# Kernel optimization log

Measured on AMD Instinct MI355X. Metric: run time of the kernel, lower is better.

Reference implementation:

```python
import jax, jax.numpy as jnp
import numpy as np

B, T, S, U, VOCAB = 32, 64, 64, 512, 65


def setup_inputs() -> dict:
    key = jax.random.key(0)
    ks = jax.random.split(key, 16)
    sd = 0.05
    return {
        "shifted_labels": jax.random.randint(ks[0], (B, T), 0, VOCAB),
        "encoder_output": jax.random.normal(ks[1], (B, S, U), jnp.float32),
        "enc_state_h": jax.random.normal(ks[2], (B, U), jnp.float32),
        "enc_state_c": jax.random.normal(ks[3], (B, U), jnp.float32),
        # decoder LSTM params (keras gate order i,f,g,o)
        "Wx": jax.random.normal(ks[4], (VOCAB, 4 * U), jnp.float32) * sd,
        "Wh": jax.random.normal(ks[5], (U, 4 * U), jnp.float32) * sd,
        "b": jnp.zeros((4 * U,), jnp.float32),
        # Bahdanau attention params
        "W1": jax.random.normal(ks[6], (U, U), jnp.float32) * sd,
        "b1": jnp.zeros((U,), jnp.float32),
        "W2": jax.random.normal(ks[7], (U, U), jnp.float32) * sd,
        "b2": jnp.zeros((U,), jnp.float32),
        "V": jax.random.normal(ks[8], (U, 1), jnp.float32) * sd,
        "bv": jnp.zeros((1,), jnp.float32),
    }


def _lstm(xz, h0, c0, Wh):
    # xz: [B, T, 4U] precomputed input projections
    def step(carry, xz_t):
        h, c = carry
        z = xz_t + h @ Wh
        i, f, g, o = jnp.split(z, 4, axis=-1)
        c = jax.nn.sigmoid(f) * c + jax.nn.sigmoid(i) * jnp.tanh(g)
        h = jax.nn.sigmoid(o) * jnp.tanh(c)
        return (h, c), h

    (_, _), hs = jax.lax.scan(step, (h0, c0), jnp.swapaxes(xz, 0, 1))
    return jnp.swapaxes(hs, 0, 1)  # [B, T, U]


def reference(shifted_labels, encoder_output, enc_state_h, enc_state_c,
              Wx, Wh, b, W1, b1, W2, b2, V, bv):
    vocab = Wx.shape[0]
    x = jax.nn.one_hot(shifted_labels, vocab, dtype=encoder_output.dtype)  # [B,T,vocab]
    xz = jnp.einsum('btv,vk->btk', x, Wx) + b                              # [B,T,4U]
    dec = _lstm(xz, enc_state_h, enc_state_c, Wh)                          # [B,T,U]
    # Bahdanau attention, vectorized over all decoder timesteps at once
    d1 = dec @ W1 + b1                # [B,T,U]
    e2 = encoder_output @ W2 + b2     # [B,S,U]  (computed once, not per step)
    score = jnp.tanh(d1[:, :, None, :] + e2[:, None, :, :]) @ V + bv  # [B,T,S,1]
    w = jax.nn.softmax(score[..., 0], axis=-1)  # softmax over encoder positions S
    return jnp.transpose(w, (0, 2, 1))          # [B,S,T] (stack axis=2 in original)
```

## Files before the change

kernel.cpp:

```cpp
#include <hip/hip_runtime.h>
#include <hip/hip_bf16.h>


#define NB 32
#define NT 64
#define NS 64
#define NU 512
#define N4U 2048
#define NV 65
#define NWG 32

typedef unsigned int u32;
typedef __bf16 bf16_t;
typedef bf16_t bf16x8 __attribute__((ext_vector_type(8)));
typedef float f32x4 __attribute__((ext_vector_type(4)));
typedef u32 u32x4 __attribute__((ext_vector_type(4)));

__device__ __forceinline__ unsigned short f2bf(float f) {
  u32 u = __builtin_bit_cast(u32, f);
  u += 0x7fffu + ((u >> 16) & 1u);
  return (unsigned short)(u >> 16);
}
__device__ __forceinline__ float bf2f(unsigned short s) {
  return __builtin_bit_cast(float, (u32)s << 16);
}
__device__ __forceinline__ u32 pk2(float a, float b) {
  return (u32)f2bf(a) | ((u32)f2bf(b) << 16);
}
__device__ __forceinline__ float sigf(float x) { return 1.0f / (1.0f + __expf(-x)); }
__device__ __forceinline__ float tanhfast(float x) {
  float e = __expf(2.0f * x);
  return 1.0f - 2.0f / (e + 1.0f);
}

__global__ __launch_bounds__(256, 1)
void lstm_kernel(const int* __restrict__ labels,
                 const float* __restrict__ h0,
                 const float* __restrict__ c0,
                 const float* __restrict__ Wx,
                 const float* __restrict__ Wh,
                 const float* __restrict__ bias,
                 const float* __restrict__ enc,
                 const float* __restrict__ W2,
                 const float* __restrict__ b2,
                 u32* __restrict__ hbuf,
                 u32* __restrict__ dec_u,
                 u32* __restrict__ flags,
                 unsigned short* __restrict__ e2_bf)
{
  __shared__ float z_buf[NB][65];
  __shared__ float c_lds[NB][16];
  __shared__ float wx_lds[NV][65];
  __shared__ unsigned char lab_lds[NB * NT];

  const int tid  = threadIdx.x;
  const int g    = blockIdx.x;
  const int wave = tid >> 6, lane = tid & 63;
  const int l15  = lane & 15, l4 = lane >> 4;

  if (g >= NWG) {
    const int r0 = (g - NWG) * 64 + wave * 16;
    const int arowE = r0 + l15;
    u32x4 afragE[16];
#pragma unroll
    for (int kt = 0; kt < 16; ++kt) {
      const float* ep = enc + arowE * NU + kt * 32 + l4 * 8;
      u32x4 t;
      t.x = pk2(ep[0], ep[1]); t.y = pk2(ep[2], ep[3]);
      t.z = pk2(ep[4], ep[5]); t.w = pk2(ep[6], ep[7]);
      afragE[kt] = t;
    }
    for (int cg = 0; cg < 8; ++cg) {
      f32x4 acc[4] = {};
      for (int kt = 0; kt < 16; ++kt) {
        bf16x8 a = __builtin_bit_cast(bf16x8, afragE[kt]);
        int k0 = kt * 32 + l4 * 8;
#pragma unroll
        for (int nt = 0; nt < 4; ++nt) {
          int col = cg * 64 + nt * 16 + l15;
          union { unsigned short us[8]; bf16x8 v; } bu;
#pragma unroll
          for (int e = 0; e < 8; ++e) bu.us[e] = f2bf(W2[(k0 + e) * NU + col]);
          acc[nt] = __builtin_amdgcn_mfma_f32_16x16x32_bf16(a, bu.v, acc[nt], 0, 0, 0);
        }
      }
#pragma unroll
      for (int nt = 0; nt < 4; ++nt) {
        int col = cg * 64 + nt * 16 + l15;
        float bc = b2[col];
#pragma unroll
        for (int ri = 0; ri < 4; ++ri)
          e2_bf[(r0 + l4 * 4 + ri) * NU + col] = f2bf(acc[nt][ri] + bc);
      }
    }
    return;
  }

  const int wm = wave >> 1, wn = wave & 1;

  for (int i = tid; i < NV * 64; i += 256) {
    int v = i >> 6, c = i & 63;
    int j = (c >> 4) * NU + g * 16 + (c & 15);
    wx_lds[v][c] = Wx[v * N4U + j] + bias[j];
  }
  for (int i = tid; i < NB * 16; i += 256) {
    int r = i >> 4, u = i & 15;
    c_lds[r][u] = c0[r * NU + g * 16 + u];
  }
  for (int i = tid; i < NB * NT; i += 256) lab_lds[i] = (unsigned char)labels[i];

  bf16x8 bfrag[16][2];
#pragma unroll
  for (int kt = 0; kt < 16; ++kt) {
#pragma unroll
    for (int nt = 0; nt < 2; ++nt) {
      int c = wn * 32 + nt * 16 + l15;
      int j = (c >> 4) * NU + g * 16 + (c & 15);
      int kb = kt * 32 + l4 * 8;
      union { unsigned short us[8]; bf16x8 v; } bu;
#pragma unroll
      for (int e = 0; e < 8; ++e) bu.us[e] = f2bf(Wh[(kb + e) * N4U + j]);
      bfrag[kt][nt] = bu.v;
    }
  }

  const int arow = wm * 16 + l15;
  u32x4 afrag[16];
#pragma unroll
  for (int kt = 0; kt < 16; ++kt) {
    const float* hp = h0 + arow * NU + kt * 32 + l4 * 8;
    u32x4 t;
    t.x = pk2(hp[0], hp[1]); t.y = pk2(hp[2], hp[3]);
    t.z = pk2(hp[4], hp[5]); t.w = pk2(hp[6], hp[7]);
    afrag[kt] = t;
  }

  const int bb = tid >> 3;
  const int u2 = (tid & 7) * 2;
  const int ci = g * 8 + (tid & 7);

  for (int s = 0; s < NT; ++s) {
    f32x4 a00 = {0.f,0.f,0.f,0.f}, a01 = a00, a10 = a00, a11 = a00;
#pragma unroll
    for (int kt = 0; kt < 16; kt += 2) {
      bf16x8 av0 = __builtin_bit_cast(bf16x8, afrag[kt]);
      bf16x8 av1 = __builtin_bit_cast(bf16x8, afrag[kt + 1]);
      a00 = __builtin_amdgcn_mfma_f32_16x16x32_bf16(av0, bfrag[kt][0],     a00, 0, 0, 0);
      a10 = __builtin_amdgcn_mfma_f32_16x16x32_bf16(av0, bfrag[kt][1],     a10, 0, 0, 0);
      a01 = __builtin_amdgcn_mfma_f32_16x16x32_bf16(av1, bfrag[kt + 1][0], a01, 0, 0, 0);
      a11 = __builtin_amdgcn_mfma_f32_16x16x32_bf16(av1, bfrag[kt + 1][1], a11, 0, 0, 0);
    }
    f32x4 acc0 = a00 + a01, acc1 = a10 + a11;

#pragma unroll
    for (int ri = 0; ri < 4; ++ri) {
      z_buf[wm * 16 + l4 * 4 + ri][wn * 32 + l15]      = acc0[ri];
      z_buf[wm * 16 + l4 * 4 + ri][wn * 32 + 16 + l15] = acc1[ri];
    }
    __syncthreads();

    int lab = lab_lds[bb * NT + s];
    float hv[2];
#pragma unroll
    for (int q = 0; q < 2; ++q) {
      int u = u2 + q;
      float zi = z_buf[bb][u]      + wx_lds[lab][u];
      float zf = z_buf[bb][16 + u] + wx_lds[lab][16 + u];
      float zg = z_buf[bb][32 + u] + wx_lds[lab][32 + u];
      float zo = z_buf[bb][48 + u] + wx_lds[lab][48 + u];
      float cc = sigf(zf) * c_lds[bb][u] + sigf(zi) * tanhfast(zg);
      c_lds[bb][u] = cc;
      hv[q] = sigf(zo) * tanhfast(cc);
    }
    u32 pkv = pk2(hv[0], hv[1]);

    if (s == NT - 1) {
      dec_u[(bb * NT + s) * 256 + ci] = pkv;
      break;
    }

    __hip_atomic_store(hbuf + (((s + 1) & 1) << 13) + bb * 256 + ci, pkv,
                       __ATOMIC_RELAXED, __HIP_MEMORY_SCOPE_AGENT);

    asm volatile("s_waitcnt vmcnt(0)" ::: "memory");
    __syncthreads();

    if (tid == 0)
      __hip_atomic_store(flags + g, (u32)(s + 1),
                         __ATOMIC_RELAXED, __HIP_MEMORY_SCOPE_AGENT);

    dec_u[(bb * NT + s) * 256 + ci] = pkv;

    {
      const u32 target = (u32)(s + 1);
      int guard = 0;
      for (;;) {
        u32 f = target;
        if (lane < NWG)
          f = __hip_atomic_load(flags + lane, __ATOMIC_RELAXED,
                                __HIP_MEMORY_SCOPE_AGENT);
        if (__all(f >= target)) break;
        if (++guard > 300000) break;
        __builtin_amdgcn_s_sleep(1);
      }
    }

    {
      const u32* ap = hbuf + (((s + 1) & 1) << 13) + arow * 256 + l4 * 4;
      asm volatile(
        "global_load_dwordx4 %0, %16, off sc0 sc1\n\t"
        "global_load_dwordx4 %1, %16, off offset:64 sc0 sc1\n\t"
        "global_load_dwordx4 %2, %16, off offset:128 sc0 sc1\n\t"
        "global_load_dwordx4 %3, %16, off offset:192 sc0 sc1\n\t"
        "global_load_dwordx4 %4, %16, off offset:256 sc0 sc1\n\t"
        "global_load_dwordx4 %5, %16, off offset:320 sc0 sc1\n\t"
        "global_load_dwordx4 %6, %16, off offset:384 sc0 sc1\n\t"
        "global_load_dwordx4 %7, %16, off offset:448 sc0 sc1\n\t"
        "global_load_dwordx4 %8, %16, off offset:512 sc0 sc1\n\t"
        "global_load_dwordx4 %9, %16, off offset:576 sc0 sc1\n\t"
        "global_load_dwordx4 %10, %16, off offset:640 sc0 sc1\n\t"
        "global_load_dwordx4 %11, %16, off offset:704 sc0 sc1\n\t"
        "global_load_dwordx4 %12, %16, off offset:768 sc0 sc1\n\t"
        "global_load_dwordx4 %13, %16, off offset:832 sc0 sc1\n\t"
        "global_load_dwordx4 %14, %16, off offset:896 sc0 sc1\n\t"
        "global_load_dwordx4 %15, %16, off offset:960 sc0 sc1\n\t"
        "s_waitcnt vmcnt(0)"
        : "=&v"(afrag[0]),  "=&v"(afrag[1]),  "=&v"(afrag[2]),  "=&v"(afrag[3]),
          "=&v"(afrag[4]),  "=&v"(afrag[5]),  "=&v"(afrag[6]),  "=&v"(afrag[7]),
          "=&v"(afrag[8]),  "=&v"(afrag[9]),  "=&v"(afrag[10]), "=&v"(afrag[11]),
          "=&v"(afrag[12]), "=&v"(afrag[13]), "=&v"(afrag[14]), "=&v"(afrag[15])
        : "v"(ap)
        : "memory");
    }
  }
}

__global__ __launch_bounds__(256, 1)
void proj_kernel(const u32* __restrict__ dec_u,
                 const float* __restrict__ W1,
                 const float* __restrict__ b1,
                 unsigned short* __restrict__ d1_bf)
{
  const int tid = threadIdx.x;
  const int wave = tid >> 6, lane = tid & 63;
  const int l15 = lane & 15, l4 = lane >> 4;
  const int w  = blockIdx.x * 4 + wave;
  const int rt = w >> 3, cg = w & 7;
  const int r0 = rt * 16;

  f32x4 acc[4] = {};
  const int arow = r0 + l15;
  for (int kt = 0; kt < 16; ++kt) {
    int k0 = kt * 32 + l4 * 8;
    bf16x8 a = __builtin_bit_cast(bf16x8,
          *reinterpret_cast<const uint4*>(dec_u + arow * 256 + (k0 >> 1)));
#pragma unroll
    for (int nt = 0; nt < 4; ++nt) {
      int col = cg * 64 + nt * 16 + l15;
      union { unsigned short us[8]; bf16x8 v; } bu;
#pragma unroll
      for (int e = 0; e < 8; ++e) bu.us[e] = f2bf(W1[(k0 + e) * NU + col]);
      acc[nt] = __builtin_amdgcn_mfma_f32_16x16x32_bf16(a, bu.v, acc[nt], 0, 0, 0);
    }
  }
#pragma unroll
  for (int nt = 0; nt < 4; ++nt) {
    int col = cg * 64 + nt * 16 + l15;
    float bc = b1[col];
#pragma unroll
    for (int ri = 0; ri < 4; ++ri) {
      int row = r0 + l4 * 4 + ri;
      d1_bf[row * NU + col] = f2bf(acc[nt][ri] + bc);
    }
  }
}

__global__ __launch_bounds__(256, 1)
void score_kernel(const unsigned short* __restrict__ d1_bf,
                  const unsigned short* __restrict__ e2_bf,
                  const float* __restrict__ V,
                  float* __restrict__ out)
{
  const int tid = threadIdx.x;
  const int wave = tid >> 6, lane = tid & 63;
  const int p = blockIdx.x * 4 + wave;
  const int bb = p >> 6, t = p & 63;

  union { uint4 q; unsigned short us[8]; } dv;
  dv.q = *reinterpret_cast<const uint4*>(d1_bf + (bb * 64 + t) * NU + lane * 8);
  float d1f[8], Vf[8];
#pragma unroll
  for (int e = 0; e < 8; ++e) { d1f[e] = bf2f(dv.us[e]); Vf[e] = V[lane * 8 + e]; }

  float sc = 0.f;
  for (int s = 0; s < NS; ++s) {
    union { uint4 q; unsigned short us[8]; } ev;
    ev.q = *reinterpret_cast<const uint4*>(e2_bf + (bb * 64 + s) * NU + lane * 8);
    float part = 0.f;
#pragma unroll
    for (int e = 0; e < 8; ++e) part += tanhfast(d1f[e] + bf2f(ev.us[e])) * Vf[e];
#pragma unroll
    for (int o = 32; o > 0; o >>= 1) part += __shfl_xor(part, o);
    sc = (lane == s) ? part : sc;
  }
  float m = sc;
#pragma unroll
  for (int o = 32; o > 0; o >>= 1) m = fmaxf(m, __shfl_xor(m, o));
  float ex = __expf(sc - m);
  float sum = ex;
#pragma unroll
  for (int o = 32; o > 0; o >>= 1) sum += __shfl_xor(sum, o);
  out[(bb * 64 + lane) * 64 + t] = ex / sum;
}

extern "C" void kernel_launch(void* const* d_in, const int* in_sizes, int n_in,
                              void* d_out, int out_size, void* d_ws, size_t ws_size,
                              hipStream_t stream)
{
  (void)in_sizes; (void)n_in; (void)out_size;
  const int*   labels = (const int*)  d_in[0];
  const float* enc    = (const float*)d_in[1];
  const float* h0     = (const float*)d_in[2];
  const float* c0     = (const float*)d_in[3];
  const float* Wx     = (const float*)d_in[4];
  const float* Wh     = (const float*)d_in[5];
  const float* bias   = (const float*)d_in[6];
  const float* W1     = (const float*)d_in[7];
  const float* b1     = (const float*)d_in[8];
  const float* W2     = (const float*)d_in[9];
  const float* b2     = (const float*)d_in[10];
  const float* V      = (const float*)d_in[11];

  char* ws = (char*)d_ws;
  const size_t OFS_HBUF = 1024;
  const size_t OFS_DEC  = 1u << 17;
  const size_t OFS_D1   = OFS_DEC + (2u << 20);
  const size_t OFS_E2   = OFS_D1  + (2u << 20);
  if (ws_size < OFS_E2 + (2u << 20)) return;

  u32* flags = (u32*)(ws);
  u32* hbuf  = (u32*)(ws + OFS_HBUF);
  u32* dec_u = (u32*)(ws + OFS_DEC);
  unsigned short* d1_bf = (unsigned short*)(ws + OFS_D1);
  unsigned short* e2_bf = (unsigned short*)(ws + OFS_E2);
  float* out = (float*)d_out;

  hipMemsetAsync(flags, 0, 256, stream);
  lstm_kernel<<<dim3(64), dim3(256), 0, stream>>>(labels, h0, c0, Wx, Wh, bias,
                                                  enc, W2, b2,
                                                  hbuf, dec_u, flags, e2_bf);
  proj_kernel<<<dim3(256), dim3(256), 0, stream>>>(dec_u, W1, b1, d1_bf);
  score_kernel<<<dim3(512), dim3(256), 0, stream>>>(d1_bf, e2_bf, V, out);
}
```

Before: 384.1 us.

## Fuse W1 projection into idle LSTM helper workgroups, overlapping it with the recurrence

The separate proj_kernel launch is removed. The 32 helper workgroups that previously only computed e2 now also compute d1 = h_t @ W1 + b1 for each timestep. They poll the per-step flags and read h_t from a full-history hbuf that replaces the double-buffered one. This hides the projection behind the serial LSTM recurrence and saves a kernel launch plus the dec_u round trip. It costs a larger workspace, extra polling traffic on the flags that could slow the critical recurrence loop, and a tail where the helpers must finish the last step after the recurrence ends.

```diff
diff --git a/kernel.cpp b/kernel.cpp
--- a/kernel.cpp
+++ b/kernel.cpp
@@ -32,6 +32,32 @@
   float e = __expf(2.0f * x);
   return 1.0f - 2.0f / (e + 1.0f);
 }
+
+#define LOAD_HSLOT(DST, AP)                                                   \
+  asm volatile(                                                               \
+    "global_load_dwordx4 %0, %16, off sc0 sc1\n\t"                            \
+    "global_load_dwordx4 %1, %16, off offset:64 sc0 sc1\n\t"                  \
+    "global_load_dwordx4 %2, %16, off offset:128 sc0 sc1\n\t"                 \
+    "global_load_dwordx4 %3, %16, off offset:192 sc0 sc1\n\t"                 \
+    "global_load_dwordx4 %4, %16, off offset:256 sc0 sc1\n\t"                 \
+    "global_load_dwordx4 %5, %16, off offset:320 sc0 sc1\n\t"                 \
+    "global_load_dwordx4 %6, %16, off offset:384 sc0 sc1\n\t"                 \
+    "global_load_dwordx4 %7, %16, off offset:448 sc0 sc1\n\t"                 \
+    "global_load_dwordx4 %8, %16, off offset:512 sc0 sc1\n\t"                 \
+    "global_load_dwordx4 %9, %16, off offset:576 sc0 sc1\n\t"                 \
+    "global_load_dwordx4 %10, %16, off offset:640 sc0 sc1\n\t"                \
+    "global_load_dwordx4 %11, %16, off offset:704 sc0 sc1\n\t"                \
+    "global_load_dwordx4 %12, %16, off offset:768 sc0 sc1\n\t"                \
+    "global_load_dwordx4 %13, %16, off offset:832 sc0 sc1\n\t"                \
+    "global_load_dwordx4 %14, %16, off offset:896 sc0 sc1\n\t"                \
+    "global_load_dwordx4 %15, %16, off offset:960 sc0 sc1\n\t"                \
+    "s_waitcnt vmcnt(0)"                                                      \
+    : "=&v"(DST[0]),  "=&v"(DST[1]),  "=&v"(DST[2]),  "=&v"(DST[3]),          \
+      "=&v"(DST[4]),  "=&v"(DST[5]),  "=&v"(DST[6]),  "=&v"(DST[7]),          \
+      "=&v"(DST[8]),  "=&v"(DST[9]),  "=&v"(DST[10]), "=&v"(DST[11]),         \
+      "=&v"(DST[12]), "=&v"(DST[13]), "=&v"(DST[14]), "=&v"(DST[15])          \
+    : "v"(AP)                                                                 \
+    : "memory")
 
 __global__ __launch_bounds__(256, 1)
 void lstm_kernel(const int* __restrict__ labels,
@@ -43,9 +69,11 @@
                  const float* __restrict__ enc,
                  const float* __restrict__ W2,
                  const float* __restrict__ b2,
+                 const float* __restrict__ W1,
+                 const float* __restrict__ b1,
                  u32* __restrict__ hbuf,
-                 u32* __restrict__ dec_u,
                  u32* __restrict__ flags,
+                 unsigned short* __restrict__ d1_bf,
                  unsigned short* __restrict__ e2_bf)
 {
   __shared__ float z_buf[NB][65];
@@ -59,38 +87,84 @@
   const int l15  = lane & 15, l4 = lane >> 4;
 
   if (g >= NWG) {
-    const int r0 = (g - NWG) * 64 + wave * 16;
-    const int arowE = r0 + l15;
-    u32x4 afragE[16];
-#pragma unroll
-    for (int kt = 0; kt < 16; ++kt) {
-      const float* ep = enc + arowE * NU + kt * 32 + l4 * 8;
-      u32x4 t;
-      t.x = pk2(ep[0], ep[1]); t.y = pk2(ep[2], ep[3]);
-      t.z = pk2(ep[4], ep[5]); t.w = pk2(ep[6], ep[7]);
-      afragE[kt] = t;
-    }
-    for (int cg = 0; cg < 8; ++cg) {
-      f32x4 acc[4] = {};
+    const int k = g - NWG;
+    {
+      const int r0 = k * 64 + wave * 16;
+      const int arowE = r0 + l15;
+      u32x4 afragE[16];
+#pragma unroll
       for (int kt = 0; kt < 16; ++kt) {
-        bf16x8 a = __builtin_bit_cast(bf16x8, afragE[kt]);
-        int k0 = kt * 32 + l4 * 8;
+        const float* ep = enc + arowE * NU + kt * 32 + l4 * 8;
+        u32x4 t;
+        t.x = pk2(ep[0], ep[1]); t.y = pk2(ep[2], ep[3]);
+        t.z = pk2(ep[4], ep[5]); t.w = pk2(ep[6], ep[7]);
+        afragE[kt] = t;
+      }
+      for (int cg = 0; cg < 8; ++cg) {
+        f32x4 acc[4] = {};
+        for (int kt = 0; kt < 16; ++kt) {
+          bf16x8 a = __builtin_bit_cast(bf16x8, afragE[kt]);
+          int k0 = kt * 32 + l4 * 8;
+#pragma unroll
+          for (int nt = 0; nt < 4; ++nt) {
+            int col = cg * 64 + nt * 16 + l15;
+            union { unsigned short us[8]; bf16x8 v; } bu;
+#pragma unroll
+            for (int e = 0; e < 8; ++e) bu.us[e] = f2bf(W2[(k0 + e) * NU + col]);
+            acc[nt] = __builtin_amdgcn_mfma_f32_16x16x32_bf16(a, bu.v, acc[nt], 0, 0, 0);
+          }
+        }
 #pragma unroll
         for (int nt = 0; nt < 4; ++nt) {
           int col = cg * 64 + nt * 16 + l15;
-          union { unsigned short us[8]; bf16x8 v; } bu;
-#pragma unroll
-          for (int e = 0; e < 8; ++e) bu.us[e] = f2bf(W2[(k0 + e) * NU + col]);
-          acc[nt] = __builtin_amdgcn_mfma_f32_16x16x32_bf16(a, bu.v, acc[nt], 0, 0, 0);
+          float bc = b2[col];
+#pragma unroll
+          for (int ri = 0; ri < 4; ++ri)
+            e2_bf[(r0 + l4 * 4 + ri) * NU + col] = f2bf(acc[nt][ri] + bc);
         }
       }
-#pragma unroll
-      for (int nt = 0; nt < 4; ++nt) {
-        int col = cg * 64 + nt * 16 + l15;
-        float bc = b2[col];
-#pragma unroll
-        for (int ri = 0; ri < 4; ++ri)
-          e2_bf[(r0 + l4 * 4 + ri) * NU + col] = f2bf(acc[nt][ri] + bc);
+    }
+
+    {
+      const int wm = wave >> 1, wn = wave & 1;
+      const int col = k * 16 + l15;
+      const float bc1 = b1[col];
+      bf16x8 bfrag1[16];
+#pragma unroll
+      for (int kt = 0; kt < 16; ++kt) {
+        int kb = kt * 32 + l4 * 8;
+        union { unsigned short us[8]; bf16x8 v; } bu;
+#pragma unroll
+        for (int e = 0; e < 8; ++e) bu.us[e] = f2bf(W1[(kb + e) * NU + col]);
+        bfrag1[kt] = bu.v;
+      }
+      const int arow1 = wm * 16 + l15;
+      for (int t = 1 + wn; t <= NT; t += 2) {
+        {
+          int guard = 0;
+          for (;;) {
+            u32 f = (u32)t;
+            if (lane < NWG)
+              f = __hip_atomic_load(flags + lane, __ATOMIC_RELAXED,
+                                    __HIP_MEMORY_SCOPE_AGENT);
+            if (__all(f >= (u32)t)) break;
+            if (++guard > 2000000) break;
+            __builtin_amdgcn_s_sleep(2);
+          }
+        }
+        u32x4 hf[16];
+        const u32* ap1 = hbuf + (size_t)t * 8192 + arow1 * 256 + l4 * 4;
+        LOAD_HSLOT(hf, ap1);
+        f32x4 acc = {0.f, 0.f, 0.f, 0.f};
+#pragma unroll
+        for (int kt = 0; kt < 16; ++kt)
+          acc = __builtin_amdgcn_mfma_f32_16x16x32_bf16(
+                  __builtin_bit_cast(bf16x8, hf[kt]), bfrag1[kt], acc, 0, 0, 0);
+#pragma unroll
+        for (int ri = 0; ri < 4; ++ri) {
+          int b = wm * 16 + l4 * 4 + ri;
+          d1_bf[(b * NT + (t - 1)) * NU + col] = f2bf(acc[ri] + bc1);
+        }
       }
     }
     return;
@@ -174,12 +248,7 @@
     }
     u32 pkv = pk2(hv[0], hv[1]);
 
-    if (s == NT - 1) {
-      dec_u[(bb * NT + s) * 256 + ci] = pkv;
-      break;
-    }
-
-    __hip_atomic_store(hbuf + (((s + 1) & 1) << 13) + bb * 256 + ci, pkv,
+    __hip_atomic_store(hbuf + (size_t)(s + 1) * 8192 + bb * 256 + ci, pkv,
                        __ATOMIC_RELAXED, __HIP_MEMORY_SCOPE_AGENT);
 
     asm volatile("s_waitcnt vmcnt(0)" ::: "memory");
@@ -189,7 +258,7 @@
       __hip_atomic_store(flags + g, (u32)(s + 1),
                          __ATOMIC_RELAXED, __HIP_MEMORY_SCOPE_AGENT);
 
-    dec_u[(bb * NT + s) * 256 + ci] = pkv;
+    if (s == NT - 1) break;
 
     {
       const u32 target = (u32)(s + 1);
@@ -206,71 +275,8 @@
     }
 
     {
-      const u32* ap = hbuf + (((s + 1) & 1) << 13) + arow * 256 + l4 * 4;
-      asm volatile(
-        "global_load_dwordx4 %0, %16, off sc0 sc1\n\t"
-        "global_load_dwordx4 %1, %16, off offset:64 sc0 sc1\n\t"
-        "global_load_dwordx4 %2, %16, off offset:128 sc0 sc1\n\t"
-        "global_load_dwordx4 %3, %16, off offset:192 sc0 sc1\n\t"
-        "global_load_dwordx4 %4, %16, off offset:256 sc0 sc1\n\t"
-        "global_load_dwordx4 %5, %16, off offset:320 sc0 sc1\n\t"
-        "global_load_dwordx4 %6, %16, off offset:384 sc0 sc1\n\t"
-        "global_load_dwordx4 %7, %16, off offset:448 sc0 sc1\n\t"
-        "global_load_dwordx4 %8, %16, off offset:512 sc0 sc1\n\t"
-        "global_load_dwordx4 %9, %16, off offset:576 sc0 sc1\n\t"
-        "global_load_dwordx4 %10, %16, off offset:640 sc0 sc1\n\t"
-        "global_load_dwordx4 %11, %16, off offset:704 sc0 sc1\n\t"
-        "global_load_dwordx4 %12, %16, off offset:768 sc0 sc1\n\t"
-        "global_load_dwordx4 %13, %16, off offset:832 sc0 sc1\n\t"
-        "global_load_dwordx4 %14, %16, off offset:896 sc0 sc1\n\t"
-        "global_load_dwordx4 %15, %16, off offset:960 sc0 sc1\n\t"
-        "s_waitcnt vmcnt(0)"
-        : "=&v"(afrag[0]),  "=&v"(afrag[1]),  "=&v"(afrag[2]),  "=&v"(afrag[3]),
-          "=&v"(afrag[4]),  "=&v"(afrag[5]),  "=&v"(afrag[6]),  "=&v"(afrag[7]),
-          "=&v"(afrag[8]),  "=&v"(afrag[9]),  "=&v"(afrag[10]), "=&v"(afrag[11]),
-          "=&v"(afrag[12]), "=&v"(afrag[13]), "=&v"(afrag[14]), "=&v"(afrag[15])
-        : "v"(ap)
-        : "memory");
-    }
-  }
-}
-
-__global__ __launch_bounds__(256, 1)
-void proj_kernel(const u32* __restrict__ dec_u,
-                 const float* __restrict__ W1,
-                 const float* __restrict__ b1,
-                 unsigned short* __restrict__ d1_bf)
-{
-  const int tid = threadIdx.x;
-  const int wave = tid >> 6, lane = tid & 63;
-  const int l15 = lane & 15, l4 = lane >> 4;
-  const int w  = blockIdx.x * 4 + wave;
-  const int rt = w >> 3, cg = w & 7;
-  const int r0 = rt * 16;
-
-  f32x4 acc[4] = {};
-  const int arow = r0 + l15;
-  for (int kt = 0; kt < 16; ++kt) {
-    int k0 = kt * 32 + l4 * 8;
-    bf16x8 a = __builtin_bit_cast(bf16x8,
-          *reinterpret_cast<const uint4*>(dec_u + arow * 256 + (k0 >> 1)));
-#pragma unroll
-    for (int nt = 0; nt < 4; ++nt) {
-      int col = cg * 64 + nt * 16 + l15;
-      union { unsigned short us[8]; bf16x8 v; } bu;
-#pragma unroll
-      for (int e = 0; e < 8; ++e) bu.us[e] = f2bf(W1[(k0 + e) * NU + col]);
-      acc[nt] = __builtin_amdgcn_mfma_f32_16x16x32_bf16(a, bu.v, acc[nt], 0, 0, 0);
-    }
-  }
-#pragma unroll
-  for (int nt = 0; nt < 4; ++nt) {
-    int col = cg * 64 + nt * 16 + l15;
-    float bc = b1[col];
-#pragma unroll
-    for (int ri = 0; ri < 4; ++ri) {
-      int row = r0 + l4 * 4 + ri;
-      d1_bf[row * NU + col] = f2bf(acc[nt][ri] + bc);
+      const u32* ap = hbuf + (size_t)(s + 1) * 8192 + arow * 256 + l4 * 4;
+      LOAD_HSLOT(afrag, ap);
     }
   }
 }
@@ -332,23 +338,21 @@
   const float* V      = (const float*)d_in[11];
 
   char* ws = (char*)d_ws;
-  const size_t OFS_HBUF = 1024;
-  const size_t OFS_DEC  = 1u << 17;
-  const size_t OFS_D1   = OFS_DEC + (2u << 20);
-  const size_t OFS_E2   = OFS_D1  + (2u << 20);
+  const size_t OFS_HB  = 32768;
+  const size_t HB_SZ   = (size_t)65 * 8192 * 4;
+  const size_t OFS_D1  = OFS_HB + HB_SZ;
+  const size_t OFS_E2  = OFS_D1 + (2u << 20);
   if (ws_size < OFS_E2 + (2u << 20)) return;
 
   u32* flags = (u32*)(ws);
-  u32* hbuf  = (u32*)(ws + OFS_HBUF);
-  u32* dec_u = (u32*)(ws + OFS_DEC);
+  u32* hbuf  = (u32*)(ws + OFS_HB);
   unsigned short* d1_bf = (unsigned short*)(ws + OFS_D1);
   unsigned short* e2_bf = (unsigned short*)(ws + OFS_E2);
   float* out = (float*)d_out;
 
   hipMemsetAsync(flags, 0, 256, stream);
   lstm_kernel<<<dim3(64), dim3(256), 0, stream>>>(labels, h0, c0, Wx, Wh, bias,
-                                                  enc, W2, b2,
-                                                  hbuf, dec_u, flags, e2_bf);
-  proj_kernel<<<dim3(256), dim3(256), 0, stream>>>(dec_u, W1, b1, d1_bf);
+                                                  enc, W2, b2, W1, b1,
+                                                  hbuf, flags, d1_bf, e2_bf);
   score_kernel<<<dim3(512), dim3(256), 0, stream>>>(d1_bf, e2_bf, V, out);
 }
```

Result: slower. 410.3 us (+6.8%).
